# Optimization experiments

Hardware: AMD Instinct MI355X
Metric: run time of the kernel (lower is better)

## Reference

```python
import jax, jax.numpy as jnp
import numpy as np

HIDDEN = 1024
NUM_HEADS = 16
HEAD_DIM = HIDDEN // NUM_HEADS
B, S = 2, 2048


def setup_inputs() -> dict:
    key = jax.random.key(0)
    ks = jax.random.split(key, 7)
    scale = 1.0 / np.sqrt(HIDDEN)
    return {
        "hidden_states": jax.random.normal(ks[0], (B, S, HIDDEN), dtype=jnp.float32),
        "attention_mask": jnp.ones((B, S), dtype=jnp.float32),
        "Wq": jax.random.normal(ks[1], (HIDDEN, HIDDEN), dtype=jnp.float32) * scale,
        "bq": jax.random.normal(ks[2], (HIDDEN,), dtype=jnp.float32) * 0.02,
        "Wk": jax.random.normal(ks[3], (HIDDEN, HIDDEN), dtype=jnp.float32) * scale,
        "bk": jax.random.normal(ks[4], (HIDDEN,), dtype=jnp.float32) * 0.02,
        "Wv": jax.random.normal(ks[5], (HIDDEN, HIDDEN), dtype=jnp.float32) * scale,
        "bv": jax.random.normal(ks[6], (HIDDEN,), dtype=jnp.float32) * 0.02,
    }


def reference(hidden_states, attention_mask, Wq, bq, Wk, bk, Wv, bv):
    # Linear projections (W stored [in, out], equivalent to torch Linear).
    q = hidden_states @ Wq + bq  # [B,S,H]
    k = hidden_states @ Wk + bk
    v = hidden_states @ Wv + bv

    def split_heads(x):  # [B,S,H] -> [B,nh,S,hd]
        return x.reshape(B, S, NUM_HEADS, HEAD_DIM).transpose(0, 2, 1, 3)

    q, k, v = split_heads(q), split_heads(k), split_heads(v)

    scores = jnp.einsum("bhqd,bhkd->bhqk", q, k) / jnp.sqrt(
        jnp.asarray(HEAD_DIM, dtype=q.dtype))
    min_val = jnp.finfo(scores.dtype).min
    ext_mask = (1.0 - attention_mask[:, None, None, :]) * min_val  # [B,1,1,S]
    scores = scores + ext_mask
    probs = jax.nn.softmax(scores, axis=-1)  # eval mode: no dropout
    ctx = jnp.einsum("bhqk,bhkd->bhqd", probs, v)
    ctx = ctx.transpose(0, 2, 1, 3).reshape(B, S, HIDDEN)
    return ctx
```

## Files before the change

kernel.cpp:

```cpp
#include <hip/hip_runtime.h>
#include <hip/hip_bf16.h>
#include <cstddef>
#include <cstdint>

#define HID 1024
#define NHEADS 16
#define HDIM 64
#define BATCH 2
#define SEQ 2048
#define MROWS (BATCH * SEQ)
#define BHT (BATCH * NHEADS)

typedef __attribute__((ext_vector_type(8))) short s8v;
typedef __attribute__((ext_vector_type(4))) float f4v;

__device__ __forceinline__ unsigned short f2bf(float x) {
    union { float f; unsigned int u; } c; c.f = x;
    return (unsigned short)((c.u + 0x7fffu + ((c.u >> 16) & 1u)) >> 16);
}
__device__ __forceinline__ unsigned int pkbf(float a, float b) {
    __hip_bfloat162 h = __float22bfloat162_rn(float2{a, b});
    union { __hip_bfloat162 v; unsigned int u; } c; c.v = h; return c.u;
}
__device__ __forceinline__ float bflo(unsigned int w) {
    union { unsigned int u; float f; } c; c.u = w << 16; return c.f;
}
__device__ __forceinline__ float bfhi(unsigned int w) {
    union { unsigned int u; float f; } c; c.u = w & 0xffff0000u; return c.f;
}

__device__ __forceinline__ void lds_load16(void* lds, const void* g) {
    __builtin_amdgcn_global_load_lds(
        (const __attribute__((address_space(1))) void*)g,
        (__attribute__((address_space(3))) void*)lds, 16, 0, 0);
}

__global__ __launch_bounds__(256) void conv_fused_kernel(
    const float* __restrict__ hs,
    const float* __restrict__ Wq, const float* __restrict__ Wk,
    const float* __restrict__ Wv,
    unsigned short* __restrict__ Ah, unsigned short* __restrict__ WTh)
{
    if (blockIdx.x < 2048) {
        const int idx = (blockIdx.x * 256 + threadIdx.x) * 8;
        float4 v0 = *(const float4*)&hs[idx];
        float4 v1 = *(const float4*)&hs[idx + 4];
        union { unsigned int w[4]; } pk;
        pk.w[0] = pkbf(v0.x, v0.y);
        pk.w[1] = pkbf(v0.z, v0.w);
        pk.w[2] = pkbf(v1.x, v1.y);
        pk.w[3] = pkbf(v1.z, v1.w);
        *(uint4*)&Ah[idx] = *(uint4*)&pk;
    } else {
        const int bid = blockIdx.x - 2048;
        const int z = bid >> 8;
        const int rem = bid & 255;
        const float* W = (z == 0) ? Wq : (z == 1) ? Wk : Wv;
        unsigned short* th = WTh + (size_t)z * HID * HID;

        __shared__ float tile[64][65];
        const int t = threadIdx.x;
        const int kb = (rem >> 4) * 64, nb = (rem & 15) * 64;
        const int c4 = (t & 15) * 4;
        const int r0 = t >> 4;

#pragma unroll
        for (int i = 0; i < 4; ++i) {
            int r = r0 + i * 16;
            float4 v = *(const float4*)&W[(size_t)(kb + r) * HID + nb + c4];
            tile[r][c4 + 0] = v.x; tile[r][c4 + 1] = v.y;
            tile[r][c4 + 2] = v.z; tile[r][c4 + 3] = v.w;
        }
        __syncthreads();
#pragma unroll
        for (int i = 0; i < 4; ++i) {
            int n = r0 + i * 16;
            union { unsigned int w[2]; unsigned long long q; } pk;
            pk.w[0] = pkbf(tile[c4 + 0][n], tile[c4 + 1][n]);
            pk.w[1] = pkbf(tile[c4 + 2][n], tile[c4 + 3][n]);
            *(unsigned long long*)&th[(size_t)(nb + n) * HID + kb + c4] = pk.q;
        }
    }
}

#define QBM 64
#define QBN 128
#define QSCALE 0.18033688011112042f

__global__ __launch_bounds__(256, 5) void qkv_mfma_kernel(
    const unsigned short* __restrict__ Ah, const unsigned short* __restrict__ WTh,
    const float* __restrict__ bq, const float* __restrict__ bk,
    const float* __restrict__ bv,
    unsigned short* __restrict__ Qg, unsigned short* __restrict__ Khi,
    unsigned short* __restrict__ VTg)
{
    const int z = blockIdx.z;
    const float* bias = (z == 0) ? bq : (z == 1) ? bk : bv;
    const unsigned short* Bh = WTh + (size_t)z * HID * HID;

    __shared__ unsigned short AS[QBM * 64];
    __shared__ unsigned short BS[QBN * 64];

    const int t = threadIdx.x;
    const int wave = t >> 6, lane = t & 63, quad = lane >> 4, l15 = lane & 15;
    const int sw = l15 & 7;
    const int rowBase = blockIdx.x * QBM;
    const int colBase = blockIdx.y * QBN;

    const int srow8 = lane >> 3;
    const int sc    = lane & 7;

    size_t goffA[2], goffB[4];
#pragma unroll
    for (int it = 0; it < 2; ++it) {
        const int row = (wave * 2 + it) * 8 + srow8;
        goffA[it] = (size_t)(rowBase + row) * HID + (sc ^ (row & 7)) * 8;
    }
#pragma unroll
    for (int it = 0; it < 4; ++it) {
        const int row = (wave * 4 + it) * 8 + srow8;
        goffB[it] = (size_t)(colBase + row) * HID + (sc ^ (row & 7)) * 8;
    }

    f4v acc[4][2];
#pragma unroll
    for (int mf = 0; mf < 4; ++mf)
#pragma unroll
        for (int nf = 0; nf < 2; ++nf) acc[mf][nf] = (f4v){0.f, 0.f, 0.f, 0.f};

    for (int kt = 0; kt < HID / 64; ++kt) {
        const int k0 = kt * 64;
        __syncthreads();
#pragma unroll
        for (int it = 0; it < 2; ++it)
            lds_load16(&AS[(wave * 2 + it) * 512], &Ah[goffA[it] + k0]);
#pragma unroll
        for (int it = 0; it < 4; ++it)
            lds_load16(&BS[(wave * 4 + it) * 512], &Bh[goffB[it] + k0]);
        __syncthreads();

#pragma unroll
        for (int kk = 0; kk < 2; ++kk) {
            const int csw = ((kk * 4 + quad) ^ sw) * 8;
            s8v af[4], bf[2];
#pragma unroll
            for (int mf = 0; mf < 4; ++mf)
                af[mf] = *(const s8v*)&AS[(mf * 16 + l15) * 64 + csw];
#pragma unroll
            for (int nf = 0; nf < 2; ++nf)
                bf[nf] = *(const s8v*)&BS[(wave * 32 + nf * 16 + l15) * 64 + csw];
#pragma unroll
            for (int mf = 0; mf < 4; ++mf)
#pragma unroll
                for (int nf = 0; nf < 2; ++nf)
                    acc[mf][nf] = __builtin_amdgcn_mfma_f32_16x16x32_bf16(af[mf], bf[nf], acc[mf][nf], 0, 0, 0);
        }
    }

#pragma unroll
    for (int nf = 0; nf < 2; ++nf) {
        const int n = colBase + wave * 32 + nf * 16 + l15;
        const float bb = bias[n];
        const int h = n >> 6, d = n & 63;
#pragma unroll
        for (int mf = 0; mf < 4; ++mf) {
            const int rw0 = rowBase + mf * 16 + quad * 4;
            const int b = rw0 >> 11;
            const int s0 = rw0 & (SEQ - 1);
            float c[4];
#pragma unroll
            for (int r = 0; r < 4; ++r) c[r] = acc[mf][nf][r] + bb;
            if (z == 0) {
#pragma unroll
                for (int r = 0; r < 4; ++r)
                    Qg[((size_t)(b * NHEADS + h) * SEQ + s0 + r) * HDIM + d] = f2bf(c[r] * QSCALE);
            } else if (z == 1) {
#pragma unroll
                for (int r = 0; r < 4; ++r)
                    Khi[((size_t)(b * NHEADS + h) * SEQ + s0 + r) * HDIM + d] = f2bf(c[r]);
            } else {
                union { unsigned int w[2]; unsigned long long q; } pk;
                pk.w[0] = pkbf(c[0], c[1]);
                pk.w[1] = pkbf(c[2], c[3]);
                *(unsigned long long*)&VTg[((size_t)(b * NHEADS + h) * HDIM + d) * SEQ + s0] = pk.q;
            }
        }
    }
}

#define BC 64

__global__ __launch_bounds__(256, 2) void attn_mfma_kernel(
    const unsigned short* __restrict__ Qg, const unsigned short* __restrict__ Khi,
    const unsigned short* __restrict__ VTg,
    const float* __restrict__ mask, float* __restrict__ out)
{
    __shared__ unsigned short Kb[2][BC * HDIM];
    __shared__ unsigned short Vb[2][BC * HDIM];
    __shared__ unsigned short Pbuf[4][32 * BC];

    const int t = threadIdx.x;
    const int wave = t >> 6, lane = t & 63, quad = lane >> 4, l15 = lane & 15;
    const int sw = l15 & 7;
    const int bh = blockIdx.x, b = bh >> 4, h = bh & (NHEADS - 1);
    const int qbase = blockIdx.y * 128 + wave * 32;

    const size_t hb = (size_t)bh * SEQ * HDIM;
    const unsigned short* kbase = Khi + hb;
    const unsigned short* vbase = VTg + hb;
    const float* mrow = mask + b * SEQ;

    s8v qh[2][2];
#pragma unroll
    for (int qf = 0; qf < 2; ++qf)
#pragma unroll
        for (int ds = 0; ds < 2; ++ds) {
            size_t off = hb + (size_t)(qbase + qf * 16 + l15) * HDIM + ds * 32 + quad * 8;
            qh[qf][ds] = *(const s8v*)&Qg[off];
        }

    f4v oacc[2][4];
#pragma unroll
    for (int qf = 0; qf < 2; ++qf)
#pragma unroll
        for (int nf = 0; nf < 4; ++nf) oacc[qf][nf] = (f4v){0.f, 0.f, 0.f, 0.f};
    float l_r[2] = {0.f, 0.f};

    const int srow8 = lane >> 3;
    const int sc    = lane & 7;
    int koff[2], voff[2];
#pragma unroll
    for (int it = 0; it < 2; ++it) {
        const int row = (wave * 2 + it) * 8 + srow8;
        const int gx = (sc ^ (row & 7)) * 8;
        koff[it] = row * HDIM + gx;
        voff[it] = row * SEQ + gx;
    }

#pragma unroll
    for (int it = 0; it < 2; ++it) {
        const int i = wave * 2 + it;
        lds_load16(&Kb[0][i * 512], kbase + koff[it]);
        lds_load16(&Vb[0][i * 512], vbase + voff[it]);
    }
    __syncthreads();

    for (int kt = 0; kt < SEQ / BC; ++kt) {
        const int cur = kt & 1;
        if (kt + 1 < SEQ / BC) {
            const int nxt = cur ^ 1;
#pragma unroll
            for (int it = 0; it < 2; ++it) {
                const int i = wave * 2 + it;
                lds_load16(&Kb[nxt][i * 512], kbase + (kt + 1) * BC * HDIM + koff[it]);
                lds_load16(&Vb[nxt][i * 512], vbase + (kt + 1) * BC + voff[it]);
            }
        }
        float4 msv[4];
#pragma unroll
        for (int mf = 0; mf < 4; ++mf)
            msv[mf] = *(const float4*)&mrow[kt * BC + mf * 16 + quad * 4];

        f4v sacc[2][4];
#pragma unroll
        for (int qf = 0; qf < 2; ++qf)
#pragma unroll
            for (int mf = 0; mf < 4; ++mf) sacc[qf][mf] = (f4v){0.f, 0.f, 0.f, 0.f};
#pragma unroll
        for (int mf = 0; mf < 4; ++mf) {
#pragma unroll
            for (int ds = 0; ds < 2; ++ds) {
                s8v kh = *(const s8v*)&Kb[cur][(mf * 16 + l15) * HDIM + (((ds * 4 + quad) ^ sw) * 8)];
#pragma unroll
                for (int qf = 0; qf < 2; ++qf)
                    sacc[qf][mf] = __builtin_amdgcn_mfma_f32_16x16x32_bf16(kh, qh[qf][ds], sacc[qf][mf], 0, 0, 0);
            }
        }

#pragma unroll
        for (int qf = 0; qf < 2; ++qf) {
            float psum = 0.f;
            const int prow = (qf * 16 + l15) * BC;
#pragma unroll
            for (int mf = 0; mf < 4; ++mf) {
                const float* mp = (const float*)&msv[mf];
                float p0 = __builtin_amdgcn_exp2f(sacc[qf][mf][0]) * mp[0];
                float p1 = __builtin_amdgcn_exp2f(sacc[qf][mf][1]) * mp[1];
                float p2 = __builtin_amdgcn_exp2f(sacc[qf][mf][2]) * mp[2];
                float p3 = __builtin_amdgcn_exp2f(sacc[qf][mf][3]) * mp[3];
                union { unsigned int w[2]; unsigned long long q; } pk;
                pk.w[0] = pkbf(p0, p1);
                pk.w[1] = pkbf(p2, p3);
                psum += bflo(pk.w[0]) + bfhi(pk.w[0]) + bflo(pk.w[1]) + bfhi(pk.w[1]);
                const int c16 = (mf * 2 + (quad >> 1)) ^ sw;
                *(unsigned long long*)&Pbuf[wave][prow + c16 * 8 + (quad & 1) * 4] = pk.q;
            }
            l_r[qf] += psum;
        }

#pragma unroll
        for (int ks = 0; ks < 2; ++ks) {
            const int csw = ((ks * 4 + quad) ^ sw) * 8;
            s8v pa0 = *(const s8v*)&Pbuf[wave][(0 * 16 + l15) * BC + csw];
            s8v pa1 = *(const s8v*)&Pbuf[wave][(1 * 16 + l15) * BC + csw];
#pragma unroll
            for (int nf = 0; nf < 4; ++nf) {
                s8v vb = *(const s8v*)&Vb[cur][(nf * 16 + l15) * BC + csw];
                oacc[0][nf] = __builtin_amdgcn_mfma_f32_16x16x32_bf16(pa0, vb, oacc[0][nf], 0, 0, 0);
                oacc[1][nf] = __builtin_amdgcn_mfma_f32_16x16x32_bf16(pa1, vb, oacc[1][nf], 0, 0, 0);
            }
        }
        __syncthreads();
    }

#pragma unroll
    for (int qf = 0; qf < 2; ++qf) {
        float v = l_r[qf];
        v += __shfl_xor(v, 16);
        v += __shfl_xor(v, 32);
        float lv[4];
#pragma unroll
        for (int r = 0; r < 4; ++r)
            lv[r] = 1.0f / __shfl(v, quad * 4 + r);
#pragma unroll
        for (int nf = 0; nf < 4; ++nf)
#pragma unroll
            for (int r = 0; r < 4; ++r) {
                int q = qbase + qf * 16 + quad * 4 + r;
                int d = nf * 16 + l15;
                out[((size_t)b * SEQ + q) * HID + h * HDIM + d] = oacc[qf][nf][r] * lv[r];
            }
    }
}

extern "C" void kernel_launch(void* const* d_in, const int* in_sizes, int n_in,
                              void* d_out, int out_size, void* d_ws, size_t ws_size,
                              hipStream_t stream) {
    const float* hs   = (const float*)d_in[0];
    const float* mask = (const float*)d_in[1];
    const float* Wq   = (const float*)d_in[2];
    const float* bq   = (const float*)d_in[3];
    const float* Wk   = (const float*)d_in[4];
    const float* bk   = (const float*)d_in[5];
    const float* Wv   = (const float*)d_in[6];
    const float* bv   = (const float*)d_in[7];
    float* out = (float*)d_out;

    const size_t N = (size_t)MROWS * HID;
    unsigned short* Qg  = (unsigned short*)d_ws;
    unsigned short* Khi = Qg + N;
    unsigned short* VTg = Qg + 2 * N;
    unsigned short* Ah  = Qg + 3 * N;
    unsigned short* WTh = Qg + 4 * N;

    conv_fused_kernel<<<2048 + 768, 256, 0, stream>>>(hs, Wq, Wk, Wv, Ah, WTh);

    dim3 g1(MROWS / QBM, HID / QBN, 3);
    qkv_mfma_kernel<<<g1, 256, 0, stream>>>(Ah, WTh, bq, bk, bv, Qg, Khi, VTg);

    dim3 g2(BHT, SEQ / 128);
    attn_mfma_kernel<<<g2, 256, 0, stream>>>(Qg, Khi, VTg, mask, out);
}
```

Baseline: 180.1 us.

## Load K/V fragments directly from global into registers with double-buffered prefetch

Removes the shared-memory staging of K and V tiles and the per-tile block barrier. Each wave now loads its MFMA fragments straight from global memory into two register sets, alternating between them so the next tile is prefetched while the current one is computed. This drops the LDS traffic and __syncthreads, but each of the four waves now fetches the same K/V data separately (4x global/L2 traffic) and uses more VGPRs, which may hurt occupancy under launch_bounds(256,2).

```diff
diff --git a/kernel.cpp b/kernel.cpp
--- a/kernel.cpp
+++ b/kernel.cpp
@@ -190,13 +190,86 @@
 
 #define BC 64
 
+struct Frags { s8v k[8]; s8v v[8]; };
+
+__device__ __forceinline__ void load_tile(
+    const unsigned short* __restrict__ kb, const unsigned short* __restrict__ vb,
+    int kt, int l15, int quad, Frags& f)
+{
+#pragma unroll
+    for (int mf = 0; mf < 4; ++mf)
+#pragma unroll
+        for (int ds = 0; ds < 2; ++ds)
+            f.k[mf * 2 + ds] = *(const s8v*)&kb[(size_t)(kt * BC + mf * 16 + l15) * HDIM + ds * 32 + quad * 8];
+#pragma unroll
+    for (int ks = 0; ks < 2; ++ks)
+#pragma unroll
+        for (int nf = 0; nf < 4; ++nf)
+            f.v[ks * 4 + nf] = *(const s8v*)&vb[(size_t)(nf * 16 + l15) * SEQ + kt * BC + ks * 32 + quad * 8];
+}
+
+__device__ __forceinline__ void attn_step(
+    const Frags& f, const float* __restrict__ mrow, int kt,
+    const s8v (&qh)[2][2], f4v (&oacc)[2][4], float (&l_r)[2],
+    unsigned short* __restrict__ pw, int quad, int l15, int sw)
+{
+    float4 msv[4];
+#pragma unroll
+    for (int mf = 0; mf < 4; ++mf)
+        msv[mf] = *(const float4*)&mrow[kt * BC + mf * 16 + quad * 4];
+
+    f4v sacc[2][4];
+#pragma unroll
+    for (int qf = 0; qf < 2; ++qf)
+#pragma unroll
+        for (int mf = 0; mf < 4; ++mf) sacc[qf][mf] = (f4v){0.f, 0.f, 0.f, 0.f};
+#pragma unroll
+    for (int mf = 0; mf < 4; ++mf)
+#pragma unroll
+        for (int ds = 0; ds < 2; ++ds)
+#pragma unroll
+            for (int qf = 0; qf < 2; ++qf)
+                sacc[qf][mf] = __builtin_amdgcn_mfma_f32_16x16x32_bf16(f.k[mf * 2 + ds], qh[qf][ds], sacc[qf][mf], 0, 0, 0);
+
+#pragma unroll
+    for (int qf = 0; qf < 2; ++qf) {
+        float psum = 0.f;
+        const int prow = (qf * 16 + l15) * BC;
+#pragma unroll
+        for (int mf = 0; mf < 4; ++mf) {
+            const float* mp = (const float*)&msv[mf];
+            float p0 = __builtin_amdgcn_exp2f(sacc[qf][mf][0]) * mp[0];
+            float p1 = __builtin_amdgcn_exp2f(sacc[qf][mf][1]) * mp[1];
+            float p2 = __builtin_amdgcn_exp2f(sacc[qf][mf][2]) * mp[2];
+            float p3 = __builtin_amdgcn_exp2f(sacc[qf][mf][3]) * mp[3];
+            union { unsigned int w[2]; unsigned long long q; } pk;
+            pk.w[0] = pkbf(p0, p1);
+            pk.w[1] = pkbf(p2, p3);
+            psum += bflo(pk.w[0]) + bfhi(pk.w[0]) + bflo(pk.w[1]) + bfhi(pk.w[1]);
+            const int c16 = (mf * 2 + (quad >> 1)) ^ sw;
+            *(unsigned long long*)&pw[prow + c16 * 8 + (quad & 1) * 4] = pk.q;
+        }
+        l_r[qf] += psum;
+    }
+
+#pragma unroll
+    for (int ks = 0; ks < 2; ++ks) {
+        const int csw = ((ks * 4 + quad) ^ sw) * 8;
+        s8v pa0 = *(const s8v*)&pw[(0 * 16 + l15) * BC + csw];
+        s8v pa1 = *(const s8v*)&pw[(1 * 16 + l15) * BC + csw];
+#pragma unroll
+        for (int nf = 0; nf < 4; ++nf) {
+            oacc[0][nf] = __builtin_amdgcn_mfma_f32_16x16x32_bf16(pa0, f.v[ks * 4 + nf], oacc[0][nf], 0, 0, 0);
+            oacc[1][nf] = __builtin_amdgcn_mfma_f32_16x16x32_bf16(pa1, f.v[ks * 4 + nf], oacc[1][nf], 0, 0, 0);
+        }
+    }
+}
+
 __global__ __launch_bounds__(256, 2) void attn_mfma_kernel(
     const unsigned short* __restrict__ Qg, const unsigned short* __restrict__ Khi,
     const unsigned short* __restrict__ VTg,
     const float* __restrict__ mask, float* __restrict__ out)
 {
-    __shared__ unsigned short Kb[2][BC * HDIM];
-    __shared__ unsigned short Vb[2][BC * HDIM];
     __shared__ unsigned short Pbuf[4][32 * BC];
 
     const int t = threadIdx.x;
@@ -209,6 +282,7 @@
     const unsigned short* kbase = Khi + hb;
     const unsigned short* vbase = VTg + hb;
     const float* mrow = mask + b * SEQ;
+    unsigned short* pw = &Pbuf[wave][0];
 
     s8v qh[2][2];
 #pragma unroll
@@ -226,91 +300,15 @@
         for (int nf = 0; nf < 4; ++nf) oacc[qf][nf] = (f4v){0.f, 0.f, 0.f, 0.f};
     float l_r[2] = {0.f, 0.f};
 
-    const int srow8 = lane >> 3;
-    const int sc    = lane & 7;
-    int koff[2], voff[2];
-#pragma unroll
-    for (int it = 0; it < 2; ++it) {
-        const int row = (wave * 2 + it) * 8 + srow8;
-        const int gx = (sc ^ (row & 7)) * 8;
-        koff[it] = row * HDIM + gx;
-        voff[it] = row * SEQ + gx;
-    }
-
-#pragma unroll
-    for (int it = 0; it < 2; ++it) {
-        const int i = wave * 2 + it;
-        lds_load16(&Kb[0][i * 512], kbase + koff[it]);
-        lds_load16(&Vb[0][i * 512], vbase + voff[it]);
-    }
-    __syncthreads();
-
-    for (int kt = 0; kt < SEQ / BC; ++kt) {
-        const int cur = kt & 1;
-        if (kt + 1 < SEQ / BC) {
-            const int nxt = cur ^ 1;
-#pragma unroll
-            for (int it = 0; it < 2; ++it) {
-                const int i = wave * 2 + it;
-                lds_load16(&Kb[nxt][i * 512], kbase + (kt + 1) * BC * HDIM + koff[it]);
-                lds_load16(&Vb[nxt][i * 512], vbase + (kt + 1) * BC + voff[it]);
-            }
-        }
-        float4 msv[4];
-#pragma unroll
-        for (int mf = 0; mf < 4; ++mf)
-            msv[mf] = *(const float4*)&mrow[kt * BC + mf * 16 + quad * 4];
-
-        f4v sacc[2][4];
-#pragma unroll
-        for (int qf = 0; qf < 2; ++qf)
-#pragma unroll
-            for (int mf = 0; mf < 4; ++mf) sacc[qf][mf] = (f4v){0.f, 0.f, 0.f, 0.f};
-#pragma unroll
-        for (int mf = 0; mf < 4; ++mf) {
-#pragma unroll
-            for (int ds = 0; ds < 2; ++ds) {
-                s8v kh = *(const s8v*)&Kb[cur][(mf * 16 + l15) * HDIM + (((ds * 4 + quad) ^ sw) * 8)];
-#pragma unroll
-                for (int qf = 0; qf < 2; ++qf)
-                    sacc[qf][mf] = __builtin_amdgcn_mfma_f32_16x16x32_bf16(kh, qh[qf][ds], sacc[qf][mf], 0, 0, 0);
-            }
-        }
-
-#pragma unroll
-        for (int qf = 0; qf < 2; ++qf) {
-            float psum = 0.f;
-            const int prow = (qf * 16 + l15) * BC;
-#pragma unroll
-            for (int mf = 0; mf < 4; ++mf) {
-                const float* mp = (const float*)&msv[mf];
-                float p0 = __builtin_amdgcn_exp2f(sacc[qf][mf][0]) * mp[0];
-                float p1 = __builtin_amdgcn_exp2f(sacc[qf][mf][1]) * mp[1];
-                float p2 = __builtin_amdgcn_exp2f(sacc[qf][mf][2]) * mp[2];
-                float p3 = __builtin_amdgcn_exp2f(sacc[qf][mf][3]) * mp[3];
-                union { unsigned int w[2]; unsigned long long q; } pk;
-                pk.w[0] = pkbf(p0, p1);
-                pk.w[1] = pkbf(p2, p3);
-                psum += bflo(pk.w[0]) + bfhi(pk.w[0]) + bflo(pk.w[1]) + bfhi(pk.w[1]);
-                const int c16 = (mf * 2 + (quad >> 1)) ^ sw;
-                *(unsigned long long*)&Pbuf[wave][prow + c16 * 8 + (quad & 1) * 4] = pk.q;
-            }
-            l_r[qf] += psum;
-        }
-
-#pragma unroll
-        for (int ks = 0; ks < 2; ++ks) {
-            const int csw = ((ks * 4 + quad) ^ sw) * 8;
-            s8v pa0 = *(const s8v*)&Pbuf[wave][(0 * 16 + l15) * BC + csw];
-            s8v pa1 = *(const s8v*)&Pbuf[wave][(1 * 16 + l15) * BC + csw];
-#pragma unroll
-            for (int nf = 0; nf < 4; ++nf) {
-                s8v vb = *(const s8v*)&Vb[cur][(nf * 16 + l15) * BC + csw];
-                oacc[0][nf] = __builtin_amdgcn_mfma_f32_16x16x32_bf16(pa0, vb, oacc[0][nf], 0, 0, 0);
-                oacc[1][nf] = __builtin_amdgcn_mfma_f32_16x16x32_bf16(pa1, vb, oacc[1][nf], 0, 0, 0);
-            }
-        }
-        __syncthreads();
+    Frags fA, fB;
+    load_tile(kbase, vbase, 0, l15, quad, fA);
+
+    for (int kt = 0; kt < SEQ / BC; kt += 2) {
+        load_tile(kbase, vbase, kt + 1, l15, quad, fB);
+        attn_step(fA, mrow, kt, qh, oacc, l_r, pw, quad, l15, sw);
+        if (kt + 2 < SEQ / BC)
+            load_tile(kbase, vbase, kt + 2, l15, quad, fA);
+        attn_step(fB, mrow, kt + 1, qh, oacc, l_r, pw, quad, l15, sw);
     }
 
 #pragma unroll
```

Measured after the change: 258.0 us. +43.3%, slower.
